# Kernel tuning notes

Hardware: AMD Instinct MI355X
Metric: run time of the kernel (lower is better)

## Reference

```python
import jax, jax.numpy as jnp
import numpy as np

N_HEADS = 16

def setup_inputs() -> dict:
    key = jax.random.key(0)
    k1, k2, k3 = jax.random.split(key, 3)
    B, T, C = 4, 2048, 1024
    x = jax.random.normal(k1, (B, T, C), dtype=jnp.float32)
    tok_mask = jnp.ones((B, T), dtype=bool)
    # weights pre-transposed to [in, out] (torch Linear stores [out, in])
    w_qkv = jax.random.normal(k2, (C, 3 * C), dtype=jnp.float32) * (C ** -0.5)
    w_proj = jax.random.normal(k3, (C, C), dtype=jnp.float32) * (C ** -0.5)
    return {"x": x, "tok_mask": tok_mask, "w_qkv": w_qkv, "w_proj": w_proj}


def reference(x, tok_mask, w_qkv, w_proj):
    B, T, C = x.shape
    H = N_HEADS
    d = C // H
    qkv = x @ w_qkv  # [B, T, 3C]
    q, k, v = jnp.split(qkv, 3, axis=-1)
    # [B, T, C] -> [B, H, T, d]
    def heads(t):
        return t.reshape(B, T, H, d).transpose(0, 2, 1, 3)
    q, k, v = heads(q), heads(k), heads(v)
    att = jnp.einsum('bhtd,bhsd->bhts', q, k) / jnp.sqrt(jnp.float32(d))
    mask = tok_mask[:, None, None, :]  # [B,1,1,T] masks keys
    causal = jnp.tril(jnp.ones((T, T), dtype=bool))[None, None]
    mask = mask & causal
    att = jnp.where(mask, att, jnp.float32(-1e9))
    att = jax.nn.softmax(att, axis=-1)
    # dropout p=0.0 -> identity (eval mode)
    y = jnp.einsum('bhts,bhsd->bhtd', att, v)  # [B,H,T,d]
    y = y.transpose(0, 2, 1, 3).reshape(B, T, C)
    return y @ w_proj
```

## Files before the change

kernel.cpp:

```cpp
#include <hip/hip_runtime.h>
#include <hip/hip_bf16.h>

typedef __attribute__((ext_vector_type(8))) short bf16x8;
typedef __attribute__((ext_vector_type(4))) float f32x4;
typedef __attribute__((ext_vector_type(8))) unsigned short u16x8;
typedef __attribute__((ext_vector_type(2))) unsigned int u32x2;

static constexpr int Tn = 2048;
static constexpr int Cc = 1024;

__device__ __forceinline__ unsigned short f2bf(float f) {
    union { float f; unsigned u; } v; v.f = f;
    unsigned u = v.u;
    u += 0x7FFFu + ((u >> 16) & 1u);
    return (unsigned short)(u >> 16);
}

__device__ __forceinline__ void gload16(const unsigned short* g, unsigned short* l) {
    __builtin_amdgcn_global_load_lds(
        (const __attribute__((address_space(1))) unsigned int*)g,
        (__attribute__((address_space(3))) unsigned int*)l, 16, 0, 0);
}

__global__ void cast_f32_bf16(const float* __restrict__ in,
                              unsigned short* __restrict__ out, int n4) {
    int i = blockIdx.x * blockDim.x + threadIdx.x;
    if (i >= n4) return;
    float4 v = ((const float4*)in)[i];
    ushort4 o;
    o.x = f2bf(v.x); o.y = f2bf(v.y); o.z = f2bf(v.z); o.w = f2bf(v.w);
    ((ushort4*)out)[i] = o;
}

__global__ void transpose_cast(const float* __restrict__ in,
                               unsigned short* __restrict__ out, int R, int N) {
    __shared__ float t[32][33];
    int c0 = blockIdx.x * 32, r0 = blockIdx.y * 32;
    int x = threadIdx.x;
    for (int yy = threadIdx.y; yy < 32; yy += 8)
        t[yy][x] = in[(size_t)(r0 + yy) * N + c0 + x];
    __syncthreads();
    for (int yy = threadIdx.y; yy < 32; yy += 8)
        out[(size_t)(c0 + yy) * R + r0 + x] = f2bf(t[x][yy]);
}

template <int OUT_BF16>
__global__ __launch_bounds__(256) void gemm_bt(const unsigned short* __restrict__ A,
                                               const unsigned short* __restrict__ Bt,
                                               void* __restrict__ Cout,
                                               int Mb, int Nb, int Kk) {
    __shared__ alignas(16) unsigned short As[128 * 64];
    __shared__ alignas(16) unsigned short Bs[128 * 64];
    const int tid = threadIdx.x;
    const int lane = tid & 63;
    const int wave = tid >> 6;
    const int wr = wave >> 1, wc = wave & 1;
    const int l15 = lane & 15;
    const int g = lane >> 4;

    const int nb = Mb * Nb;
    const int bid = blockIdx.x;
    const int swz = (bid & 7) * (nb >> 3) + (bid >> 3);
    const int bx = swz % Nb, by = swz / Nb;
    const int brow = by * 128, bcol = bx * 128;
    const int Nn = Nb * 128;

    const int lr = lane >> 3;
    const int sc = 8 * ((lane & 7) ^ lr);
    const unsigned short* Abase = &A[(size_t)(brow + wave * 32 + lr) * Kk + sc];
    const unsigned short* Bbase = &Bt[(size_t)(bcol + wave * 32 + lr) * Kk + sc];

    f32x4 acc[4][4] = {};

    for (int k0 = 0; k0 < Kk; k0 += 64) {
        __syncthreads();
#pragma unroll
        for (int j = 0; j < 4; ++j) {
            gload16(Abase + (size_t)(j * 8) * Kk + k0, &As[(wave * 32 + j * 8) * 64]);
            gload16(Bbase + (size_t)(j * 8) * Kk + k0, &Bs[(wave * 32 + j * 8) * 64]);
        }
        __syncthreads();

#pragma unroll
        for (int dk = 0; dk < 2; ++dk) {
            const int cs = 8 * ((dk * 4 + g) ^ (l15 & 7));
            bf16x8 af[4], bfr[4];
#pragma unroll
            for (int m = 0; m < 4; ++m)
                af[m] = *(const bf16x8*)&As[(wr * 64 + m * 16 + l15) * 64 + cs];
#pragma unroll
            for (int n = 0; n < 4; ++n)
                bfr[n] = *(const bf16x8*)&Bs[(wc * 64 + n * 16 + l15) * 64 + cs];
#pragma unroll
            for (int m = 0; m < 4; ++m)
#pragma unroll
                for (int n = 0; n < 4; ++n)
                    acc[m][n] = __builtin_amdgcn_mfma_f32_16x16x32_bf16(af[m], bfr[n], acc[m][n], 0, 0, 0);
        }
    }

    const float qs = (OUT_BF16 && bcol < 1024) ? 0.18033688011112042f : 1.0f;

#pragma unroll
    for (int m = 0; m < 4; ++m) {
        int row = brow + wr * 64 + m * 16 + g * 4;
#pragma unroll
        for (int n = 0; n < 4; ++n) {
            int col = bcol + wc * 64 + n * 16 + l15;
#pragma unroll
            for (int i = 0; i < 4; ++i) {
                float v = acc[m][n][i];
                if (OUT_BF16)
                    ((unsigned short*)Cout)[(size_t)(row + i) * Nn + col] = f2bf(v * qs);
                else
                    ((float*)Cout)[(size_t)(row + i) * Nn + col] = v;
            }
        }
    }
}

__global__ __launch_bounds__(256) void attn_fwd(const unsigned short* __restrict__ qkv,
                                                unsigned short* __restrict__ yb) {
    __shared__ alignas(16) unsigned short Ks[2][4096];
    __shared__ alignas(16) unsigned int   Vt[2][64][34];
    __shared__ alignas(16) unsigned int   Ps[4][32][34];

    const int tid = threadIdx.x;
    const int lane = tid & 63;
    const int w = tid >> 6;
    const int l15 = lane & 15;
    const int g = lane >> 4;

    const int bid = blockIdx.x;
    const int xcd = bid & 7;
    const int u = bid >> 3;
    const int bh = xcd * 8 + (u & 7);
    const int qb = 15 - (u >> 3);
    const int b = bh >> 4, h = bh & 15;
    const int rb = b * Tn;
    const int q0 = qb * 128;
    const int colQ = h * 64, colK = Cc + h * 64, colV = 2 * Cc + h * 64;

    const int kr = lane >> 3;
    const unsigned short* ksrc =
        &qkv[(size_t)(rb + 8 * w + kr) * 3072 + colK + 8 * ((lane & 7) ^ kr)];
    const size_t krow32 = (size_t)32 * 3072;

    const int rp = tid >> 3;
    const int l15v = rp & 15, hv = (rp >> 4) & 1;
    const int vcg = (tid & 7) * 8;
    const int wcol = l15v * 2 + hv;

    bf16x8 aq[2][2];
#pragma unroll
    for (int m = 0; m < 2; ++m) {
        const unsigned short* qrow =
            &qkv[(size_t)(rb + q0 + w * 32 + m * 16 + l15) * 3072 + colQ];
        aq[m][0] = *(const bf16x8*)&qrow[g * 8];
        aq[m][1] = *(const bf16x8*)&qrow[32 + g * 8];
    }

    f32x4 accy[2][4] = {};
    float lsum[2][4] = {};
    const int kswz = 8 * (l15 & 7);

#define ATILE(P, S0, DG) do {                                                     \
    const unsigned short* kb = &Ks[P][0];                                         \
    f32x4 accs[2][4] = {};                                                        \
    __builtin_amdgcn_s_setprio(1);                                                \
    _Pragma("unroll")                                                             \
    for (int dk = 0; dk < 2; ++dk) {                                              \
        _Pragma("unroll")                                                         \
        for (int n = 0; n < 4; ++n) {                                             \
            bf16x8 bk = *(const bf16x8*)&kb[(n * 16 + l15) * 64 +                 \
                                            ((dk * 32 + g * 8) ^ kswz)];          \
            accs[0][n] = __builtin_amdgcn_mfma_f32_16x16x32_bf16(aq[0][dk], bk, accs[0][n], 0, 0, 0); \
            accs[1][n] = __builtin_amdgcn_mfma_f32_16x16x32_bf16(aq[1][dk], bk, accs[1][n], 0, 0, 0); \
        }                                                                         \
    }                                                                             \
    __builtin_amdgcn_s_setprio(0);                                                \
    _Pragma("unroll")                                                             \
    for (int m = 0; m < 2; ++m) {                                                 \
        _Pragma("unroll")                                                         \
        for (int i = 0; i < 4; ++i) {                                             \
            float pe[4];                                                          \
            _Pragma("unroll")                                                     \
            for (int n = 0; n < 4; ++n) {                                         \
                float v = exp2f(accs[m][n][i]);                                   \
                if (DG) { if ((S0) + n * 16 + l15 >                               \
                              q0 + w * 32 + m * 16 + g * 4 + i) v = 0.f; }        \
                pe[n] = v; lsum[m][i] += v;                                       \
            }                                                                     \
            u32x2 pk;                                                             \
            asm("v_cvt_pk_bf16_f32 %0, %1, %2" : "=v"(pk.x) : "v"(pe[0]), "v"(pe[1])); \
            asm("v_cvt_pk_bf16_f32 %0, %1, %2" : "=v"(pk.y) : "v"(pe[2]), "v"(pe[3])); \
            *(u32x2*)&Ps[w][m * 16 + g * 4 + i][l15 * 2] = pk;                    \
        }                                                                         \
    }                                                                             \
    __builtin_amdgcn_s_setprio(1);                                                \
    _Pragma("unroll")                                                             \
    for (int ks = 0; ks < 2; ++ks) {                                              \
        bf16x8 pa0 = *(const bf16x8*)&Ps[w][l15][ks * 16 + g * 4];                \
        bf16x8 pa1 = *(const bf16x8*)&Ps[w][16 + l15][ks * 16 + g * 4];           \
        _Pragma("unroll")                                                         \
        for (int n = 0; n < 4; ++n) {                                             \
            bf16x8 bv = *(const bf16x8*)&Vt[P][n * 16 + l15][ks * 16 + g * 4];    \
            accy[0][n] = __builtin_amdgcn_mfma_f32_16x16x32_bf16(pa0, bv, accy[0][n], 0, 0, 0); \
            accy[1][n] = __builtin_amdgcn_mfma_f32_16x16x32_bf16(pa1, bv, accy[1][n], 0, 0, 0); \
        }                                                                         \
    }                                                                             \
    __builtin_amdgcn_s_setprio(0);                                                \
} while (0)

    const int nt = 2 * qb + 2;
    const size_t step = (size_t)64 * 3072;

    gload16(ksrc, &Ks[0][w * 512]);
    gload16(ksrc + krow32, &Ks[0][2048 + w * 512]);
    {
        const unsigned short* vb = &qkv[(size_t)rb * 3072 + colV + vcg];
        u16x8 v0 = *(const u16x8*)&vb[(size_t)(hv * 32 + l15v) * 3072];
        u16x8 v1 = *(const u16x8*)&vb[(size_t)(hv * 32 + 16 + l15v) * 3072];
#pragma unroll
        for (int j = 0; j < 8; ++j)
            Vt[0][vcg + j][wcol] = (unsigned)(unsigned short)v0[j] |
                                   ((unsigned)(unsigned short)v1[j] << 16);
    }
    __syncthreads();

    int p = 0;
    for (int t = 0; t < nt - 2; ++t) {
        gload16(ksrc + (size_t)(t + 1) * step, &Ks[p ^ 1][w * 512]);
        gload16(ksrc + (size_t)(t + 1) * step + krow32, &Ks[p ^ 1][2048 + w * 512]);
        const unsigned short* vb = &qkv[(size_t)(rb + (t + 1) * 64) * 3072 + colV + vcg];
        u16x8 v0 = *(const u16x8*)&vb[(size_t)(hv * 32 + l15v) * 3072];
        u16x8 v1 = *(const u16x8*)&vb[(size_t)(hv * 32 + 16 + l15v) * 3072];

        ATILE(p, t * 64, 0);

#pragma unroll
        for (int j = 0; j < 8; ++j)
            Vt[p ^ 1][vcg + j][wcol] = (unsigned)(unsigned short)v0[j] |
                                       ((unsigned)(unsigned short)v1[j] << 16);
        __syncthreads();
        p ^= 1;
    }
    {
        const int t = nt - 2;
        gload16(ksrc + (size_t)(t + 1) * step, &Ks[p ^ 1][w * 512]);
        gload16(ksrc + (size_t)(t + 1) * step + krow32, &Ks[p ^ 1][2048 + w * 512]);
        const unsigned short* vb = &qkv[(size_t)(rb + (t + 1) * 64) * 3072 + colV + vcg];
        u16x8 v0 = *(const u16x8*)&vb[(size_t)(hv * 32 + l15v) * 3072];
        u16x8 v1 = *(const u16x8*)&vb[(size_t)(hv * 32 + 16 + l15v) * 3072];

        ATILE(p, t * 64, 1);

#pragma unroll
        for (int j = 0; j < 8; ++j)
            Vt[p ^ 1][vcg + j][wcol] = (unsigned)(unsigned short)v0[j] |
                                       ((unsigned)(unsigned short)v1[j] << 16);
        __syncthreads();
        p ^= 1;
        if (w >= 2) {
            ATILE(p, (t + 1) * 64, 1);
        }
    }
#undef ATILE

#pragma unroll
    for (int m = 0; m < 2; ++m)
#pragma unroll
        for (int i = 0; i < 4; ++i) {
            float ls = lsum[m][i];
#pragma unroll
            for (int off = 1; off < 16; off <<= 1)
                ls += __shfl_xor(ls, off, 64);
            lsum[m][i] = ls;
        }
#pragma unroll
    for (int m = 0; m < 2; ++m)
#pragma unroll
        for (int n = 0; n < 4; ++n)
#pragma unroll
            for (int i = 0; i < 4; ++i) {
                int row = rb + q0 + w * 32 + m * 16 + g * 4 + i;
                int col = h * 64 + n * 16 + l15;
                yb[(size_t)row * 1024 + col] = f2bf(accy[m][n][i] / lsum[m][i]);
            }
}

extern "C" void kernel_launch(void* const* d_in, const int* in_sizes, int n_in,
                              void* d_out, int out_size, void* d_ws, size_t ws_size,
                              hipStream_t stream) {
    const float* x      = (const float*)d_in[0];
    const float* w_qkv  = (const float*)d_in[2];
    const float* w_proj = (const float*)d_in[3];
    float* out = (float*)d_out;

    const int M = 4 * 2048;
    unsigned short* xb     = (unsigned short*)d_ws;
    unsigned short* wqkvT  = xb + (size_t)M * 1024;
    unsigned short* wprojT = wqkvT + (size_t)3072 * 1024;
    unsigned short* qkvb   = wprojT + (size_t)1024 * 1024;
    unsigned short* yb     = qkvb + (size_t)M * 3072;

    {
        int n4 = (M * 1024) / 4;
        cast_f32_bf16<<<(n4 + 255) / 256, 256, 0, stream>>>(x, xb, n4);
    }
    transpose_cast<<<dim3(3072 / 32, 1024 / 32), dim3(32, 8), 0, stream>>>(w_qkv, wqkvT, 1024, 3072);
    transpose_cast<<<dim3(1024 / 32, 1024 / 32), dim3(32, 8), 0, stream>>>(w_proj, wprojT, 1024, 1024);

    gemm_bt<1><<<64 * 24, 256, 0, stream>>>(xb, wqkvT, qkvb, 64, 24, 1024);

    attn_fwd<<<1024, 256, 0, stream>>>(qkvb, yb);

    gemm_bt<0><<<64 * 8, 256, 0, stream>>>(yb, wprojT, out, 64, 8, 1024);
}
```

Baseline: 183.8 us.

## Double attention query block to 256 rows with 8 waves sharing K/V tiles

The attention kernel now runs 512-thread blocks of 8 waves, each block handling 256 query rows instead of 128, so every staged K/V tile is reused by twice as many waves and half as many blocks reload K/V. K staging now uses one gload per thread and V staging is limited to the first 256 threads. The causal tail is handled generically per wave using part/diagonal predicates, and block ordering pairs long and short query blocks. The trade-off is fewer blocks (512), more wave imbalance near the diagonal, and larger shared memory per block.

```diff
diff --git a/kernel.cpp b/kernel.cpp
--- a/kernel.cpp
+++ b/kernel.cpp
@@ -119,11 +119,11 @@
     }
 }
 
-__global__ __launch_bounds__(256) void attn_fwd(const unsigned short* __restrict__ qkv,
-                                                unsigned short* __restrict__ yb) {
+__global__ __launch_bounds__(512, 4) void attn_fwd(const unsigned short* __restrict__ qkv,
+                                                   unsigned short* __restrict__ yb) {
     __shared__ alignas(16) unsigned short Ks[2][4096];
     __shared__ alignas(16) unsigned int   Vt[2][64][34];
-    __shared__ alignas(16) unsigned int   Ps[4][32][34];
+    __shared__ alignas(16) unsigned int   Ps[8][32][34];
 
     const int tid = threadIdx.x;
     const int lane = tid & 63;
@@ -133,23 +133,26 @@
 
     const int bid = blockIdx.x;
     const int xcd = bid & 7;
-    const int u = bid >> 3;
-    const int bh = xcd * 8 + (u & 7);
-    const int qb = 15 - (u >> 3);
+    const int j = bid >> 3;
+    const int bhs = j & 7;
+    const int ord = j >> 3;
+    const int qb = (ord < 4) ? (7 - ord) : (ord - 4);
+    const int bh = xcd * 8 + bhs;
     const int b = bh >> 4, h = bh & 15;
     const int rb = b * Tn;
-    const int q0 = qb * 128;
+    const int q0 = qb * 256;
+    const int nt = 4 * qb + 4;
     const int colQ = h * 64, colK = Cc + h * 64, colV = 2 * Cc + h * 64;
 
     const int kr = lane >> 3;
     const unsigned short* ksrc =
         &qkv[(size_t)(rb + 8 * w + kr) * 3072 + colK + 8 * ((lane & 7) ^ kr)];
-    const size_t krow32 = (size_t)32 * 3072;
 
     const int rp = tid >> 3;
     const int l15v = rp & 15, hv = (rp >> 4) & 1;
     const int vcg = (tid & 7) * 8;
     const int wcol = l15v * 2 + hv;
+    const bool vstage = (tid < 256);
 
     bf16x8 aq[2][2];
 #pragma unroll
@@ -212,58 +215,47 @@
     __builtin_amdgcn_s_setprio(0);                                                \
 } while (0)
 
-    const int nt = 2 * qb + 2;
     const size_t step = (size_t)64 * 3072;
 
     gload16(ksrc, &Ks[0][w * 512]);
-    gload16(ksrc + krow32, &Ks[0][2048 + w * 512]);
-    {
+    if (vstage) {
         const unsigned short* vb = &qkv[(size_t)rb * 3072 + colV + vcg];
         u16x8 v0 = *(const u16x8*)&vb[(size_t)(hv * 32 + l15v) * 3072];
         u16x8 v1 = *(const u16x8*)&vb[(size_t)(hv * 32 + 16 + l15v) * 3072];
 #pragma unroll
-        for (int j = 0; j < 8; ++j)
-            Vt[0][vcg + j][wcol] = (unsigned)(unsigned short)v0[j] |
-                                   ((unsigned)(unsigned short)v1[j] << 16);
+        for (int j2 = 0; j2 < 8; ++j2)
+            Vt[0][vcg + j2][wcol] = (unsigned)(unsigned short)v0[j2] |
+                                    ((unsigned)(unsigned short)v1[j2] << 16);
     }
     __syncthreads();
 
     int p = 0;
-    for (int t = 0; t < nt - 2; ++t) {
-        gload16(ksrc + (size_t)(t + 1) * step, &Ks[p ^ 1][w * 512]);
-        gload16(ksrc + (size_t)(t + 1) * step + krow32, &Ks[p ^ 1][2048 + w * 512]);
-        const unsigned short* vb = &qkv[(size_t)(rb + (t + 1) * 64) * 3072 + colV + vcg];
-        u16x8 v0 = *(const u16x8*)&vb[(size_t)(hv * 32 + l15v) * 3072];
-        u16x8 v1 = *(const u16x8*)&vb[(size_t)(hv * 32 + 16 + l15v) * 3072];
-
-        ATILE(p, t * 64, 0);
-
-#pragma unroll
-        for (int j = 0; j < 8; ++j)
-            Vt[p ^ 1][vcg + j][wcol] = (unsigned)(unsigned short)v0[j] |
-                                       ((unsigned)(unsigned short)v1[j] << 16);
+    for (int t = 0; t < nt; ++t) {
+        const bool pre = (t + 1 < nt);
+        u16x8 v0, v1;
+        if (pre) {
+            gload16(ksrc + (size_t)(t + 1) * step, &Ks[p ^ 1][w * 512]);
+            if (vstage) {
+                const unsigned short* vb =
+                    &qkv[(size_t)(rb + (t + 1) * 64) * 3072 + colV + vcg];
+                v0 = *(const u16x8*)&vb[(size_t)(hv * 32 + l15v) * 3072];
+                v1 = *(const u16x8*)&vb[(size_t)(hv * 32 + 16 + l15v) * 3072];
+            }
+        }
+        const int t4 = t - 4 * qb;
+        const bool part = (t4 < 0) || (w >= 2 * t4);
+        const bool dg = (t4 >= 0) && (w <= 2 * t4 + 1);
+        if (part) {
+            ATILE(p, t * 64, dg);
+        }
+        if (pre && vstage) {
+#pragma unroll
+            for (int j2 = 0; j2 < 8; ++j2)
+                Vt[p ^ 1][vcg + j2][wcol] = (unsigned)(unsigned short)v0[j2] |
+                                            ((unsigned)(unsigned short)v1[j2] << 16);
+        }
         __syncthreads();
         p ^= 1;
-    }
-    {
-        const int t = nt - 2;
-        gload16(ksrc + (size_t)(t + 1) * step, &Ks[p ^ 1][w * 512]);
-        gload16(ksrc + (size_t)(t + 1) * step + krow32, &Ks[p ^ 1][2048 + w * 512]);
-        const unsigned short* vb = &qkv[(size_t)(rb + (t + 1) * 64) * 3072 + colV + vcg];
-        u16x8 v0 = *(const u16x8*)&vb[(size_t)(hv * 32 + l15v) * 3072];
-        u16x8 v1 = *(const u16x8*)&vb[(size_t)(hv * 32 + 16 + l15v) * 3072];
-
-        ATILE(p, t * 64, 1);
-
-#pragma unroll
-        for (int j = 0; j < 8; ++j)
-            Vt[p ^ 1][vcg + j][wcol] = (unsigned)(unsigned short)v0[j] |
-                                       ((unsigned)(unsigned short)v1[j] << 16);
-        __syncthreads();
-        p ^= 1;
-        if (w >= 2) {
-            ATILE(p, (t + 1) * 64, 1);
-        }
     }
 #undef ATILE
 
@@ -313,7 +305,7 @@
 
     gemm_bt<1><<<64 * 24, 256, 0, stream>>>(xb, wqkvT, qkvb, 64, 24, 1024);
 
-    attn_fwd<<<1024, 256, 0, stream>>>(qkvb, yb);
+    attn_fwd<<<512, 512, 0, stream>>>(qkvb, yb);
 
     gemm_bt<0><<<64 * 8, 256, 0, stream>>>(yb, wprojT, out, 64, 8, 1024);
 }
```

New measurement: 209.0 us. 1.14x slower.
